# Performance work log

Measured on AMD Instinct MI355X. Metric: run time of the kernel, lower is better.

Reference implementation:

```python
import jax, jax.numpy as jnp
import numpy as np

TIME_LEN = 8
JOINT_NUM = 22
SEQ = TIME_LEN * JOINT_NUM  # 176
H_NUM = 8
H_DIM = 32
NEG_BIG = -9e15


def _temporal_mask():
    # ones everywhere, except block-diagonal joint x joint blocks zeroed, plus identity
    m = np.ones((SEQ, SEQ), dtype=np.float32)
    for i in range(TIME_LEN):
        m[i * JOINT_NUM:(i + 1) * JOINT_NUM, i * JOINT_NUM:(i + 1) * JOINT_NUM] = 0.0
    spatial = 1.0 - m
    temporal = m + np.eye(SEQ, dtype=np.float32)
    return jnp.asarray(temporal), jnp.asarray(spatial)


def setup_inputs() -> dict:
    key = jax.random.key(0)
    ks = jax.random.split(key, 4)
    B, S, D_in = 256, SEQ, 128
    D_model = H_NUM * H_DIM
    s = 1.0 / np.sqrt(D_in)
    return {
        "x": jax.random.normal(ks[0], (B, S, D_in), dtype=jnp.float32),
        "Wq": jax.random.normal(ks[1], (D_in, D_model), dtype=jnp.float32) * s,
        "bq": jnp.zeros((D_model,), dtype=jnp.float32),
        "Wk": jax.random.normal(ks[2], (D_in, D_model), dtype=jnp.float32) * s,
        "bk": jnp.zeros((D_model,), dtype=jnp.float32),
        "Wv": jax.random.normal(ks[3], (D_in, D_model), dtype=jnp.float32) * s,
        "bv": jnp.zeros((D_model,), dtype=jnp.float32),
    }


def reference(x, Wq, bq, Wk, bk, Wv, bv):
    B = x.shape[0]
    mask, _ = _temporal_mask()  # att_type == 'temporal'

    def split_heads(t):  # [B,S,H*D] -> [B,H,S,D]
        return t.reshape(B, SEQ, H_NUM, H_DIM).transpose(0, 2, 1, 3)

    q = split_heads(x @ Wq + bq)
    k = split_heads(x @ Wk + bk)
    v = split_heads(jax.nn.relu(x @ Wv + bv))  # value map has ReLU

    scores = jnp.einsum("bhsd,bhtd->bhst", q, k) / jnp.sqrt(jnp.float32(H_DIM))
    scores = scores * mask + (1.0 - mask) * NEG_BIG
    att = jax.nn.softmax(scores, axis=-1)
    out = jnp.einsum("bhst,bhtd->bhsd", att, v)
    return out.transpose(0, 2, 1, 3).reshape(B, SEQ, H_NUM * H_DIM)
```

## Files before the change

kernel.cpp:

```cpp
#include <hip/hip_runtime.h>


#define SEQ    176
#define HD     32
#define DIN    128
#define DMODEL 256

typedef unsigned short ushort_t;
typedef __attribute__((ext_vector_type(8))) short short8;
typedef __attribute__((ext_vector_type(4))) short short4v;
typedef __attribute__((ext_vector_type(4))) float float4v;
typedef __attribute__((ext_vector_type(4))) unsigned short ushort4v;

#define WS_WT 0u
#define WS_X  196608u

#define SMEM_TOTAL 39936
#define OFF_KS 13056
#define OFF_VT 27136
#define KS_B   7040
#define VT_B   6400

__device__ __forceinline__ ushort_t f2bf(float f) {
    union { float f; unsigned int u; } cv; cv.f = f;
    unsigned int u = cv.u;
    unsigned int rb = 0x7FFFu + ((u >> 16) & 1u);
    return (ushort_t)((u + rb) >> 16);
}

__global__ __launch_bounds__(256)
void k0_conv(const float* __restrict__ x,
             const float* __restrict__ Wq, const float* __restrict__ Wk,
             const float* __restrict__ Wv,
             ushort_t* __restrict__ WT, ushort_t* __restrict__ X16)
{
    int bid = blockIdx.x;
    if (bid < 5632) {
        int f4 = bid * 256 + threadIdx.x;
        float4 v = reinterpret_cast<const float4*>(x)[f4];
        ushort4v o;
        o.x = f2bf(v.x); o.y = f2bf(v.y); o.z = f2bf(v.z); o.w = f2bf(v.w);
        reinterpret_cast<ushort4v*>(X16)[f4] = o;
    } else {
        int idx = (bid - 5632) * 256 + threadIdx.x;
        int e = idx * 4;
        int mat = e >> 15, h = (e >> 12) & 7, n = (e >> 7) & 31, k = e & 127;
        const float* W = (mat == 0) ? Wq : ((mat == 1) ? Wk : Wv);
        ushort4v o;
        o.x = f2bf(W[(k + 0) * DMODEL + h * HD + n]);
        o.y = f2bf(W[(k + 1) * DMODEL + h * HD + n]);
        o.z = f2bf(W[(k + 2) * DMODEL + h * HD + n]);
        o.w = f2bf(W[(k + 3) * DMODEL + h * HD + n]);
        reinterpret_cast<ushort4v*>(WT)[idx] = o;
    }
}

__global__ __launch_bounds__(704, 6)
void k1_attn(const ushort_t* __restrict__ X16, const ushort_t* __restrict__ WT,
             const float* __restrict__ bq, const float* __restrict__ bk,
             const float* __restrict__ bv, float* __restrict__ out)
{
    __shared__ ushort_t smem[SMEM_TOTAL];
    ushort_t* WS = smem;
    ushort_t* KS = smem + OFF_KS;
    ushort_t* VT = smem + OFF_VT;

    const int tid  = threadIdx.x;
    const int lane = tid & 63;
    const int w    = tid >> 6;
    const int c    = lane & 15;
    const int q    = lane >> 4;
    const int b0   = (blockIdx.x >> 3) * 2;
    const int h    = blockIdx.x & 7;

#pragma unroll
    for (int it = 0; it < 3; ++it) {
        int c8 = tid + it * 704;
        if (c8 < 1536) {
            int mat = c8 >> 9, rem = c8 & 511, n = rem >> 4, kc = rem & 15;
            short8 v = *reinterpret_cast<const short8*>(
                WT + (size_t)(((mat * 8 + h) * 32 + n) * 128 + kc * 8));
            *reinterpret_cast<short8*>(WS + (mat * 32 + n) * 136 + kc * 8) = v;
        }
    }
    if (tid < 512) {
        int bb = tid >> 8, rem = tid & 255;
        int row = rem >> 3, ch = rem & 7;
        short4v z = {0, 0, 0, 0};
        *reinterpret_cast<short4v*>(VT + bb * VT_B + row * 200 + 160 + ch * 4) = z;
    }
    __syncthreads();

    short8 xf[2][4];
#pragma unroll
    for (int bb = 0; bb < 2; ++bb) {
        const ushort_t* xr = X16 + ((size_t)(b0 + bb) * SEQ + w * 16 + c) * DIN;
#pragma unroll
        for (int kk = 0; kk < 4; ++kk)
            xf[bb][kk] = *reinterpret_cast<const short8*>(xr + kk * 32 + q * 8);
    }

    const float qscale = 0.17677669529663687f * 1.4426950408889634f;
    short8 qf8[2];
    const int skv = (c >> 2) * 8 + (c & 3);
    const int svt = (w >> 1) * 32 + (c >> 2) * 8 + (w & 1) * 4 + (c & 3);

#pragma unroll
    for (int jj = 0; jj < 6; ++jj) {
        const int mat = jj >> 1, nt = jj & 1;
        const ushort_t* wrow = WS + (mat * 32 + nt * 16 + c) * 136 + q * 8;
        short8 wf[4];
#pragma unroll
        for (int kk = 0; kk < 4; ++kk)
            wf[kk] = *reinterpret_cast<const short8*>(wrow + kk * 32);

#pragma unroll
        for (int bb = 0; bb < 2; ++bb) {
            float4v acc = {0.f, 0.f, 0.f, 0.f};
            if (mat == 1) {
#pragma unroll
                for (int kk = 0; kk < 4; ++kk)
                    acc = __builtin_amdgcn_mfma_f32_16x16x32_bf16(xf[bb][kk], wf[kk], acc, 0, 0, 0);
            } else {
#pragma unroll
                for (int kk = 0; kk < 4; ++kk)
                    acc = __builtin_amdgcn_mfma_f32_16x16x32_bf16(wf[kk], xf[bb][kk], acc, 0, 0, 0);
            }
            if (mat == 0) {
                float4 bb4 = *reinterpret_cast<const float4*>(bq + h * HD + nt * 16 + q * 4);
                qf8[bb][nt * 4 + 0] = (short)f2bf((acc[0] + bb4.x) * qscale);
                qf8[bb][nt * 4 + 1] = (short)f2bf((acc[1] + bb4.y) * qscale);
                qf8[bb][nt * 4 + 2] = (short)f2bf((acc[2] + bb4.z) * qscale);
                qf8[bb][nt * 4 + 3] = (short)f2bf((acc[3] + bb4.w) * qscale);
            } else if (mat == 1) {
                float bia = bk[h * HD + nt * 16 + c];
                ushort_t* ksb = KS + bb * KS_B;
#pragma unroll
                for (int r = 0; r < 4; ++r)
                    ksb[(w * 16 + q * 4 + r) * 40 + skv + nt * 4] = f2bf(acc[r] + bia);
            } else {
                float4 bb4 = *reinterpret_cast<const float4*>(bv + h * HD + nt * 16 + q * 4);
                ushort_t* vtb = VT + bb * VT_B;
#pragma unroll
                for (int r = 0; r < 4; ++r) {
                    float bias_r = (r == 0) ? bb4.x : (r == 1) ? bb4.y : (r == 2) ? bb4.z : bb4.w;
                    float v = acc[r] + bias_r;
                    v = v > 0.f ? v : 0.f;
                    vtb[(nt * 16 + q * 4 + r) * 200 + svt] = f2bf(v);
                }
            }
        }
    }
    __syncthreads();

    const int t_row = w * 16 + c;
    const int lo = (t_row / 22) * 22;

#pragma unroll
    for (int bb = 0; bb < 2; ++bb) {
        const ushort_t* KSb = KS + bb * KS_B;
        const ushort_t* VTb = VT + bb * VT_B;
        float su = 0.f;
        short8 pf[6];
        pf[5] = (short8){0, 0, 0, 0, 0, 0, 0, 0};
#pragma unroll
        for (int n = 0; n < 11; ++n) {
            short8 kf = *reinterpret_cast<const short8*>(KSb + (n * 16 + c) * 40 + q * 8);
            float4v s = {0.f, 0.f, 0.f, 0.f};
            s = __builtin_amdgcn_mfma_f32_16x16x32_bf16(kf, qf8[bb], s, 0, 0, 0);
#pragma unroll
            for (int r = 0; r < 4; ++r) {
                int tp = n * 16 + q * 4 + r;
                float sv = (((unsigned)(tp - lo) < 22u) && (tp != t_row)) ? -1e30f : s[r];
                float e = __builtin_amdgcn_exp2f(sv);
                su += e;
                pf[n >> 1][(n & 1) * 4 + r] = (short)f2bf(e);
            }
        }
        su += __shfl_xor(su, 16, 64);
        su += __shfl_xor(su, 32, 64);
        const float invs = 1.0f / su;

        float* ob = out + ((size_t)(b0 + bb) * SEQ + t_row) * DMODEL + h * HD;
#pragma unroll
        for (int mt = 0; mt < 2; ++mt) {
            const ushort_t* vrow = VTb + (mt * 16 + c) * 200;
            float4v o = {0.f, 0.f, 0.f, 0.f};
#pragma unroll
            for (int g = 0; g < 6; ++g) {
                short8 vf = *reinterpret_cast<const short8*>(vrow + g * 32 + q * 8);
                o = __builtin_amdgcn_mfma_f32_16x16x32_bf16(vf, pf[g], o, 0, 0, 0);
            }
            float4 st;
            st.x = o[0] * invs; st.y = o[1] * invs;
            st.z = o[2] * invs; st.w = o[3] * invs;
            *reinterpret_cast<float4*>(ob + mt * 16 + q * 4) = st;
        }
    }
}

extern "C" void kernel_launch(void* const* d_in, const int* in_sizes, int n_in,
                              void* d_out, int out_size, void* d_ws, size_t ws_size,
                              hipStream_t stream) {
    const float* x  = (const float*)d_in[0];
    const float* Wq = (const float*)d_in[1];
    const float* bq = (const float*)d_in[2];
    const float* Wk = (const float*)d_in[3];
    const float* bk = (const float*)d_in[4];
    const float* Wv = (const float*)d_in[5];
    const float* bv = (const float*)d_in[6];
    float* out = (float*)d_out;

    char* ws = (char*)d_ws;
    ushort_t* WT  = (ushort_t*)(ws + WS_WT);
    ushort_t* X16 = (ushort_t*)(ws + WS_X);

    k0_conv<<<dim3(5728), dim3(256), 0, stream>>>(x, Wq, Wk, Wv, WT, X16);
    k1_attn<<<dim3(1024), dim3(704), 0, stream>>>(X16, WT, bq, bk, bv, out);
}
```

Measured before the change: 135.9 us.

## Fuse x bf16 conversion into attention kernel, drop separate X16 pass

```diff
diff --git a/kernel.cpp b/kernel.cpp
--- a/kernel.cpp
+++ b/kernel.cpp
@@ -13,7 +13,6 @@
 typedef __attribute__((ext_vector_type(4))) unsigned short ushort4v;
 
 #define WS_WT 0u
-#define WS_X  196608u
 
 #define SMEM_TOTAL 39936
 #define OFF_KS 13056
@@ -21,42 +20,35 @@
 #define KS_B   7040
 #define VT_B   6400
 
-__device__ __forceinline__ ushort_t f2bf(float f) {
+__device__ __forceinline__ ushort_t f2bf_rtne(float f) {
     union { float f; unsigned int u; } cv; cv.f = f;
     unsigned int u = cv.u;
     unsigned int rb = 0x7FFFu + ((u >> 16) & 1u);
     return (ushort_t)((u + rb) >> 16);
 }
+__device__ __forceinline__ ushort_t f2bf(float f) {
+    union { float f; unsigned int u; } cv; cv.f = f;
+    return (ushort_t)((cv.u + 0x8000u) >> 16);
+}
 
 __global__ __launch_bounds__(256)
-void k0_conv(const float* __restrict__ x,
-             const float* __restrict__ Wq, const float* __restrict__ Wk,
-             const float* __restrict__ Wv,
-             ushort_t* __restrict__ WT, ushort_t* __restrict__ X16)
+void k0_conv(const float* __restrict__ Wq, const float* __restrict__ Wk,
+             const float* __restrict__ Wv, ushort_t* __restrict__ WT)
 {
-    int bid = blockIdx.x;
-    if (bid < 5632) {
-        int f4 = bid * 256 + threadIdx.x;
-        float4 v = reinterpret_cast<const float4*>(x)[f4];
-        ushort4v o;
-        o.x = f2bf(v.x); o.y = f2bf(v.y); o.z = f2bf(v.z); o.w = f2bf(v.w);
-        reinterpret_cast<ushort4v*>(X16)[f4] = o;
-    } else {
-        int idx = (bid - 5632) * 256 + threadIdx.x;
-        int e = idx * 4;
-        int mat = e >> 15, h = (e >> 12) & 7, n = (e >> 7) & 31, k = e & 127;
-        const float* W = (mat == 0) ? Wq : ((mat == 1) ? Wk : Wv);
-        ushort4v o;
-        o.x = f2bf(W[(k + 0) * DMODEL + h * HD + n]);
-        o.y = f2bf(W[(k + 1) * DMODEL + h * HD + n]);
-        o.z = f2bf(W[(k + 2) * DMODEL + h * HD + n]);
-        o.w = f2bf(W[(k + 3) * DMODEL + h * HD + n]);
-        reinterpret_cast<ushort4v*>(WT)[idx] = o;
-    }
+    int idx = blockIdx.x * 256 + threadIdx.x;
+    int e = idx * 4;
+    int mat = e >> 15, h = (e >> 12) & 7, n = (e >> 7) & 31, k = e & 127;
+    const float* W = (mat == 0) ? Wq : ((mat == 1) ? Wk : Wv);
+    ushort4v o;
+    o.x = f2bf_rtne(W[(k + 0) * DMODEL + h * HD + n]);
+    o.y = f2bf_rtne(W[(k + 1) * DMODEL + h * HD + n]);
+    o.z = f2bf_rtne(W[(k + 2) * DMODEL + h * HD + n]);
+    o.w = f2bf_rtne(W[(k + 3) * DMODEL + h * HD + n]);
+    reinterpret_cast<ushort4v*>(WT)[idx] = o;
 }
 
 __global__ __launch_bounds__(704, 6)
-void k1_attn(const ushort_t* __restrict__ X16, const ushort_t* __restrict__ WT,
+void k1_attn(const float* __restrict__ x, const ushort_t* __restrict__ WT,
              const float* __restrict__ bq, const float* __restrict__ bk,
              const float* __restrict__ bv, float* __restrict__ out)
 {
@@ -94,10 +86,18 @@
     short8 xf[2][4];
 #pragma unroll
     for (int bb = 0; bb < 2; ++bb) {
-        const ushort_t* xr = X16 + ((size_t)(b0 + bb) * SEQ + w * 16 + c) * DIN;
-#pragma unroll
-        for (int kk = 0; kk < 4; ++kk)
-            xf[bb][kk] = *reinterpret_cast<const short8*>(xr + kk * 32 + q * 8);
+        const float* xr = x + ((size_t)(b0 + bb) * SEQ + w * 16 + c) * DIN;
+#pragma unroll
+        for (int kk = 0; kk < 4; ++kk) {
+            float4 a0 = *reinterpret_cast<const float4*>(xr + kk * 32 + q * 8);
+            float4 a1 = *reinterpret_cast<const float4*>(xr + kk * 32 + q * 8 + 4);
+            short8 v;
+            v[0] = (short)f2bf(a0.x); v[1] = (short)f2bf(a0.y);
+            v[2] = (short)f2bf(a0.z); v[3] = (short)f2bf(a0.w);
+            v[4] = (short)f2bf(a1.x); v[5] = (short)f2bf(a1.y);
+            v[6] = (short)f2bf(a1.z); v[7] = (short)f2bf(a1.w);
+            xf[bb][kk] = v;
+        }
     }
 
     const float qscale = 0.17677669529663687f * 1.4426950408889634f;
@@ -143,7 +143,8 @@
                 ushort_t* vtb = VT + bb * VT_B;
 #pragma unroll
                 for (int r = 0; r < 4; ++r) {
-                    float bias_r = (r == 0) ? bb4.x : (r == 1) ? bb4.y : (r == 2) ? bb4.z : bb4.w;
+                    float bias_r = (r == 0) ? bb4.x : (r == 1) ? bb4.y
+                                  : (r == 2) ? bb4.z : bb4.w;
                     float v = acc[r] + bias_r;
                     v = v > 0.f ? v : 0.f;
                     vtb[(nt * 16 + q * 4 + r) * 200 + svt] = f2bf(v);
@@ -211,10 +212,8 @@
     const float* bv = (const float*)d_in[6];
     float* out = (float*)d_out;
 
-    char* ws = (char*)d_ws;
-    ushort_t* WT  = (ushort_t*)(ws + WS_WT);
-    ushort_t* X16 = (ushort_t*)(ws + WS_X);
-
-    k0_conv<<<dim3(5728), dim3(256), 0, stream>>>(x, Wq, Wk, Wv, WT, X16);
-    k1_attn<<<dim3(1024), dim3(704), 0, stream>>>(X16, WT, bq, bk, bv, out);
-}
+    ushort_t* WT = (ushort_t*)((char*)d_ws + WS_WT);
+
+    k0_conv<<<dim3(96), dim3(256), 0, stream>>>(Wq, Wk, Wv, WT);
+    k1_attn<<<dim3(1024), dim3(704), 0, stream>>>(x, WT, bq, bk, bv, out);
+}
```

New measurement: 146.5 us. +7.8%, slower.
